# Kernel tuning notes

Hardware: AMD Instinct MI355X
Metric: run time of the kernel (lower is better)

## Reference

```python
import jax, jax.numpy as jnp
import numpy as np
from math import sqrt

B, T, C = 2, 2048, 2048
H = 16
NOPE, ROPE, VD, LORA = 128, 64, 128, 512
QK = NOPE + ROPE  # 192
EPS = 1e-6


def _make_freq_cis(T, rope_dim):
    inv = 1.0 / (10000.0 ** (np.arange(0, rope_dim, 2, dtype=np.float32) / rope_dim))
    t = np.arange(T, dtype=np.float32)
    ang = np.outer(t, inv)  # [T, rope_dim/2]
    return jnp.asarray(np.stack([np.cos(ang), np.sin(ang)], -1))  # [T, rope_dim/2, 2]


def setup_inputs() -> dict:
    key = jax.random.key(0)
    ks = jax.random.split(key, 6)
    x = jax.random.normal(ks[0], (B, T, C), jnp.float32)
    freq_cis = _make_freq_cis(T, ROPE)
    causal = jnp.where(jnp.tril(jnp.ones((T, T), bool)), 0.0, -1e9).astype(jnp.float32)
    Wq = jax.random.normal(ks[1], (C, H * QK), jnp.float32) * (1.0 / sqrt(C))
    Wckv = jax.random.normal(ks[2], (C, LORA + ROPE), jnp.float32) * (1.0 / sqrt(C))
    kv_norm_w = jnp.ones((LORA,), jnp.float32)
    Wdkv = jax.random.normal(ks[3], (LORA, H * (NOPE + VD)), jnp.float32) * (1.0 / sqrt(LORA))
    Wproj = jax.random.normal(ks[4], (H * VD, C), jnp.float32) * (1.0 / sqrt(H * VD))
    return {"x": x, "freq_cis": freq_cis, "mask": causal, "window": causal,
            "Wq": Wq, "Wckv": Wckv, "kv_norm_w": kv_norm_w, "Wdkv": Wdkv,
            "Wproj": Wproj, "start_pos": 0}


def apply_rope(x, freq_cis):
    # x: [B, T, h, D]; freq_cis: [T, D/2, 2]
    b, t, h, d = x.shape
    xr = x.reshape(b, t, h, d // 2, 2)
    fc = freq_cis.reshape(1, t, 1, d // 2, 2)
    real = xr[..., 0] * fc[..., 0] - xr[..., 1] * fc[..., 1]
    imag = xr[..., 1] * fc[..., 0] + xr[..., 0] * fc[..., 1]
    return jnp.stack([real, imag], -1).reshape(b, t, h, d)


def rms_norm(x, w, eps=EPS):
    return x * jax.lax.rsqrt(jnp.mean(x * x, -1, keepdims=True) + eps) * w


def reference(x, freq_cis, mask, window, Wq, Wckv, kv_norm_w, Wdkv, Wproj, start_pos):
    del window, start_pos  # Global attention, no KV cache (prefill)
    b, t, _ = x.shape
    q = (x @ Wq).reshape(b, t, H, QK)
    q_nope, q_rope = q[..., :NOPE], q[..., NOPE:]
    q_rope = apply_rope(q_rope, freq_cis)

    ckv = x @ Wckv  # [B, T, LORA+ROPE]
    kv_lat, k_rope = ckv[..., :LORA], ckv[..., LORA:]
    k_rope = apply_rope(k_rope.reshape(b, t, 1, ROPE), freq_cis)  # [B,T,1,ROPE]

    kv = rms_norm(kv_lat, kv_norm_w) @ Wdkv  # [B, T, H*(NOPE+VD)]
    kv = kv.reshape(b, t, H, NOPE + VD)
    k_nope, v = kv[..., :NOPE], kv[..., NOPE:]

    q = jnp.concatenate([q_nope, q_rope], -1)                                   # [B,T,H,QK]
    k = jnp.concatenate([k_nope, jnp.broadcast_to(k_rope, (b, t, H, ROPE))], -1)

    scale = 1.0 / sqrt(QK)
    atten = jnp.einsum('bqhd,bkhd->bhqk', q, k) * scale + mask  # [B,H,T,T]
    atten = jax.nn.softmax(atten, -1)
    out = jnp.einsum('bhqk,bkhd->bqhd', atten, v).reshape(b, t, H * VD)
    return out @ Wproj
```

## Files before the change

### kernel.cpp

```cpp
#include <hip/hip_runtime.h>
#include <hip/hip_bf16.h>
#include <math.h>


typedef short bf16x8 __attribute__((ext_vector_type(8)));
typedef float f32x4 __attribute__((ext_vector_type(4)));
typedef float f32x16 __attribute__((ext_vector_type(16)));

#define MFMA16(a, b, c) __builtin_amdgcn_mfma_f32_16x16x32_bf16(a, b, c, 0, 0, 0)
#define MFMA32(a, b, c) __builtin_amdgcn_mfma_f32_32x32x16_bf16(a, b, c, 0, 0, 0)

__device__ __forceinline__ short f2bf(float f) {
  union { float f; unsigned u; } v; v.f = f;
  unsigned r = v.u + 0x7fffu + ((v.u >> 16) & 1u);
  return (short)(r >> 16);
}
__device__ __forceinline__ float bf2f(short s) {
  union { unsigned u; float f; } v;
  v.u = ((unsigned)(unsigned short)s) << 16;
  return v.f;
}
__device__ __forceinline__ unsigned cvtpk(float a, float b) {
  unsigned r;
  asm("v_cvt_pk_bf16_f32 %0, %1, %2" : "=v"(r) : "v"(a), "v"(b));
  return r;
}
__device__ __forceinline__ void gl16(const void* g, void* l) {
  __builtin_amdgcn_global_load_lds(
      (const __attribute__((address_space(1))) unsigned int*)g,
      (__attribute__((address_space(3))) unsigned int*)l, 16, 0, 0);
}
#define CFENCE() asm volatile("" ::: "memory")
#define HWBAR()  do { CFENCE(); __builtin_amdgcn_s_barrier(); CFENCE(); } while (0)

__global__ __launch_bounds__(256) void cvt_k(const float* __restrict__ in,
                                             short* __restrict__ out, int n) {
  int i = (blockIdx.x * 256 + threadIdx.x) * 8;
  if (i >= n) return;
  float4 a = *(const float4*)(in + i);
  float4 b = *(const float4*)(in + i + 4);
  bf16x8 o;
  o[0] = f2bf(a.x); o[1] = f2bf(a.y); o[2] = f2bf(a.z); o[3] = f2bf(a.w);
  o[4] = f2bf(b.x); o[5] = f2bf(b.y); o[6] = f2bf(b.z); o[7] = f2bf(b.w);
  *(bf16x8*)(out + i) = o;
}

__global__ __launch_bounds__(256) void tcvt_k(const float* __restrict__ W,
                                              short* __restrict__ out,
                                              int K, int N, int Np, int row_off) {
  __shared__ float tile[32][33];
  int k0 = blockIdx.x * 32, n0 = blockIdx.y * 32;
  int tx = threadIdx.x & 31, ty = threadIdx.x >> 5;
#pragma unroll
  for (int j = 0; j < 4; j++) {
    int k = k0 + ty + j * 8, n = n0 + tx;
    tile[ty + j * 8][tx] = (n < N) ? W[(size_t)k * N + n] : 0.f;
  }
  __syncthreads();
#pragma unroll
  for (int j = 0; j < 4; j++) {
    int n = n0 + ty + j * 8;
    out[(size_t)(row_off + n) * K + k0 + tx] = f2bf(tile[tx][ty + j * 8]);
  }
}

template <int MODE, int BM, int BN, int SGL>
__global__ __launch_bounds__(512, 2) void gemm8_k(const short* __restrict__ A,
                                                  const short* __restrict__ Bt,
                                                  void* __restrict__ C1,
                                                  void* __restrict__ C2,
                                                  int M, int N, int K, int nbx) {
  constexpr int FM = BM / 32;
  constexpr int FN = BN / 64;
  constexpr int XCH = (BM * 4) / 512;
  constexpr int YCH = (BN * 4) / 512;
  __shared__ short lX[3][BM * 32];
  __shared__ short lY[3][BN * 32];

  const int nwg = gridDim.x;
  const int cpx = nwg >> 3;
  const int swz = (blockIdx.x & 7) * cpx + (blockIdx.x >> 3);
  const int bx = swz % nbx, by = swz / nbx;
  const int m0 = bx * BM, n0 = by * BN;
  const int tid = threadIdx.x, lane = tid & 63, wave = tid >> 6;
  const int wm = wave >> 2, wn = wave & 3;
  const int l15 = lane & 15, l4 = lane >> 4;
  const int nt = K >> 5;

  auto stage = [&](int t) {
    int kk = t << 5;
    short* bX = &lX[t % 3][0];
    short* bY = &lY[t % 3][0];
#pragma unroll
    for (int c = 0; c < XCH; c++) {
      int idx = c * 512 + tid;
      int row = idx >> 2, seg = idx & 3;
      gl16(A + (size_t)(m0 + row) * K + kk + ((seg ^ ((row >> 1) & 3)) << 3),
           bX + idx * 8);
    }
#pragma unroll
    for (int c = 0; c < YCH; c++) {
      int idx = c * 512 + tid;
      int row = idx >> 2, seg = idx & 3;
      gl16(Bt + (size_t)(n0 + row) * K + kk + ((seg ^ ((row >> 1) & 3)) << 3),
           bY + idx * 8);
    }
  };

  f32x4 zero = {0.f, 0.f, 0.f, 0.f};
  f32x4 acc[FM][FN];
#pragma unroll
  for (int i = 0; i < FM; i++)
#pragma unroll
    for (int j = 0; j < FN; j++) acc[i][j] = zero;

  stage(0);
  stage(1);
  if constexpr (SGL == 4) asm volatile("s_waitcnt vmcnt(4)" ::: "memory");
  else                    asm volatile("s_waitcnt vmcnt(3)" ::: "memory");
  HWBAR();

  for (int t = 0; t < nt; t++) {
    const short* bX = &lX[t % 3][0];
    const short* bY = &lY[t % 3][0];
    bf16x8 xf[FM / 2], yf[FN];
#pragma unroll
    for (int i = 0; i < FM / 2; i++) {
      int row = wm * (BM / 2) + i * 16 + l15;
      xf[i] = *(const bf16x8*)&bX[row * 32 + ((l4 ^ ((row >> 1) & 3)) << 3)];
    }
#pragma unroll
    for (int j = 0; j < FN; j++) {
      int row = wn * (BN / 4) + j * 16 + l15;
      yf[j] = *(const bf16x8*)&bY[row * 32 + ((l4 ^ ((row >> 1) & 3)) << 3)];
    }
    bool st = (t + 2 < nt);
    if (st) stage(t + 2);
    HWBAR();
    __builtin_amdgcn_sched_barrier(0);
    __builtin_amdgcn_s_setprio(1);
#pragma unroll
    for (int i = 0; i < FM / 2; i++)
#pragma unroll
      for (int j = 0; j < FN; j++) acc[i][j] = MFMA16(xf[i], yf[j], acc[i][j]);
    __builtin_amdgcn_s_setprio(0);
    bf16x8 xg[FM / 2];
#pragma unroll
    for (int i = 0; i < FM / 2; i++) {
      int row = wm * (BM / 2) + (FM / 2 + i) * 16 + l15;
      xg[i] = *(const bf16x8*)&bX[row * 32 + ((l4 ^ ((row >> 1) & 3)) << 3)];
    }
    if (st) {
      if constexpr (SGL == 4) asm volatile("s_waitcnt vmcnt(4) lgkmcnt(0)" ::: "memory");
      else                    asm volatile("s_waitcnt vmcnt(3) lgkmcnt(0)" ::: "memory");
    } else {
      asm volatile("s_waitcnt vmcnt(0) lgkmcnt(0)" ::: "memory");
    }
    HWBAR();
    __builtin_amdgcn_sched_barrier(0);
    __builtin_amdgcn_s_setprio(1);
#pragma unroll
    for (int i = 0; i < FM / 2; i++)
#pragma unroll
      for (int j = 0; j < FN; j++)
        acc[FM / 2 + i][j] = MFMA16(xg[i], yf[j], acc[FM / 2 + i][j]);
    __builtin_amdgcn_s_setprio(0);
  }

#pragma unroll
  for (int i = 0; i < FM; i++) {
#pragma unroll
    for (int j = 0; j < FN; j++) {
#pragma unroll
      for (int r = 0; r < 4; r++) {
        int m = m0 + wm * (BM / 2) + i * 16 + l4 * 4 + r;
        int n = n0 + wn * (BN / 4) + j * 16 + l15;
        if (n >= N) continue;
        float v = acc[i][j][r];
        if (MODE == 0) {
          ((short*)C1)[(size_t)m * N + n] = f2bf(v);
        } else if (MODE == 1) {
          ((float*)C1)[(size_t)m * N + n] = v;
        } else {
          int bb = m >> 11, t2 = m & 2047, hh = n >> 8, c = n & 255;
          if (c < 128)
            ((short*)C1)[((size_t)(bb * 16 + hh) * 2048 + t2) * 192 + c] = f2bf(v);
          else
            ((short*)C2)[((size_t)(bb * 16 + hh) * 128 + (c - 128)) * 2048 + t2] = f2bf(v);
        }
      }
    }
  }
}

__global__ __launch_bounds__(256) void rmsnorm_k(const short* __restrict__ qc,
                                                 const float* __restrict__ w,
                                                 short* __restrict__ out) {
  int row = blockIdx.x * 4 + (threadIdx.x >> 6);
  int lane = threadIdx.x & 63;
  const short* src = qc + (size_t)row * 3712 + 3072 + lane * 8;
  bf16x8 v = *(const bf16x8*)src;
  float f[8];
  float ss = 0.f;
#pragma unroll
  for (int j = 0; j < 8; j++) { f[j] = bf2f(v[j]); ss += f[j] * f[j]; }
#pragma unroll
  for (int m = 1; m < 64; m <<= 1) ss += __shfl_xor(ss, m);
  float r = rsqrtf(ss * (1.f / 512.f) + 1e-6f);
  bf16x8 o;
#pragma unroll
  for (int j = 0; j < 8; j++) o[j] = f2bf(f[j] * r * w[lane * 8 + j]);
  *(bf16x8*)(out + (size_t)row * 512 + lane * 8) = o;
}

__global__ __launch_bounds__(256) void qrope_k(const short* __restrict__ qc,
                                               const float* __restrict__ freq,
                                               short* __restrict__ q_all) {
  int row = blockIdx.x * 4 + (threadIdx.x >> 6);
  int lane = threadIdx.x & 63;
  int b = row >> 15, h = (row >> 11) & 15, t = row & 2047;
  const short* src = qc + (size_t)(b * 2048 + t) * 3712 + h * 192;
  short* dst = q_all + (size_t)row * 192;
  const float scale = 0.10411756f;
  dst[lane] = f2bf(bf2f(src[lane]) * scale);
  dst[lane + 64] = f2bf(bf2f(src[lane + 64]) * scale);
  int p = lane >> 1;
  float c = freq[t * 64 + p * 2], s = freq[t * 64 + p * 2 + 1];
  float x0 = bf2f(src[128 + 2 * p]), x1 = bf2f(src[128 + 2 * p + 1]);
  float v = (lane & 1) ? (x1 * c + x0 * s) : (x0 * c - x1 * s);
  dst[128 + lane] = f2bf(v * scale);
}

__global__ __launch_bounds__(64) void krope_k(const short* __restrict__ qc,
                                              const float* __restrict__ freq,
                                              short* __restrict__ k_all) {
  int bt = blockIdx.x;
  int lane = threadIdx.x;
  int b = bt >> 11, t = bt & 2047;
  const short* src = qc + (size_t)bt * 3712 + 3584;
  int p = lane >> 1;
  float c = freq[t * 64 + p * 2], s = freq[t * 64 + p * 2 + 1];
  float x0 = bf2f(src[2 * p]), x1 = bf2f(src[2 * p + 1]);
  float v = (lane & 1) ? (x1 * c + x0 * s) : (x0 * c - x1 * s);
  short vb = f2bf(v);
#pragma unroll
  for (int h = 0; h < 16; h++)
    k_all[((size_t)(b * 16 + h) * 2048 + t) * 192 + 128 + lane] = vb;
}

__device__ __forceinline__ void stage_kv4(const short* __restrict__ Kp,
                                          const short* __restrict__ VT,
                                          short* kb, short* vb, int kt, int tid) {
#pragma unroll
  for (int i = 0; i < 3; i++) {
    int idx = i * 256 + tid;
    int row = idx / 24, seg = idx % 24;
    gl16(Kp + (size_t)(kt + row) * 192 + ((seg ^ (row & 7)) << 3), kb + idx * 8);
  }
#pragma unroll
  for (int i = 0; i < 2; i++) {
    int v = i * 256 + tid;
    int row = v >> 2, seg = v & 3;
    gl16(VT + (size_t)row * 2048 + kt + ((seg ^ ((row >> 1) & 3)) << 3), vb + v * 8);
  }
}

__global__ __launch_bounds__(256) void attn_k(const short* __restrict__ q_all,
                                              const short* __restrict__ k_all,
                                              const short* __restrict__ vt,
                                              short* __restrict__ attn_out) {
  __shared__ short kbuf[2][32 * 192];
  __shared__ short vbuf[2][128 * 32];
  int bh = blockIdx.x;
  int b = bh >> 4, h = bh & 15;
  int col = gridDim.y - 1 - blockIdx.y;
  int tid = threadIdx.x;
  int wave = tid >> 6, lane = tid & 63;
  int l31 = lane & 31, hi = lane >> 5;
  int qw = col * 128 + wave * 32;
  int qrow = qw + l31;
  const short* Q = q_all + ((size_t)bh * 2048 + qrow) * 192;
  const short* Kp = k_all + (size_t)bh * 2048 * 192;
  const short* VT = vt + (size_t)bh * 128 * 2048;
  int sig = (l31 & 19) | ((l31 >> 1) & 4) | ((l31 << 1) & 8);
  int s7 = sig & 7;

  bf16x8 qf[12];
#pragma unroll
  for (int kb = 0; kb < 12; kb++)
    qf[kb] = *(const bf16x8*)(Q + kb * 16 + hi * 8);

  f32x16 o[4];
#pragma unroll
  for (int vb = 0; vb < 4; vb++)
#pragma unroll
    for (int r = 0; r < 16; r++) o[vb][r] = 0.f;
  f32x16 sInit;
#pragma unroll
  for (int r = 0; r < 16; r++) sInit[r] = -28.8539f;
  float lsum = 0.f;

  const int kend = col * 128 + 128;

  stage_kv4(Kp, VT, kbuf[0], vbuf[0], 0, tid);
  __syncthreads();

  for (int kt = 0; kt < kend; kt += 32) {
    int cur = (kt >> 5) & 1;
    if (kt + 32 < kend)
      stage_kv4(Kp, VT, kbuf[cur ^ 1], vbuf[cur ^ 1], kt + 32, tid);

    if (kt < qw + 32) {
      f32x16 sc = sInit;
#pragma unroll
      for (int kb = 0; kb < 12; kb++) {
        int c = 2 * kb + hi;
        bf16x8 kf = *(const bf16x8*)&kbuf[cur][sig * 192 + ((c ^ s7) << 3)];
        sc = MFMA32(kf, qf[kb], sc);
      }
      unsigned pw[8];
      if (kt + 32 <= qw) {
#pragma unroll
        for (int r2 = 0; r2 < 8; r2++) {
          float pa = exp2f(sc[2 * r2]);
          float pb = exp2f(sc[2 * r2 + 1]);
          lsum += pa + pb;
          pw[r2] = cvtpk(pa, pb);
        }
      } else {
#pragma unroll
        for (int r2 = 0; r2 < 8; r2++) {
          int r = 2 * r2;
          int key = kt + (r & 3) + 4 * ((r >> 2) & 1) + 8 * hi + 16 * (r >> 3);
          float va = (key <= qrow) ? sc[r] : -1e30f;
          float vb2 = (key + 1 <= qrow) ? sc[r + 1] : -1e30f;
          float pa = exp2f(va);
          float pb = exp2f(vb2);
          lsum += pa + pb;
          pw[r2] = cvtpk(pa, pb);
        }
      }
      union { unsigned u[4]; bf16x8 v; } p0, p1;
#pragma unroll
      for (int w = 0; w < 4; w++) { p0.u[w] = pw[w]; p1.u[w] = pw[4 + w]; }
#pragma unroll
      for (int vb = 0; vb < 4; vb++) {
        int vcol = vb * 32 + l31;
        int sw = (vcol >> 1) & 3;
        bf16x8 vf0 = *(const bf16x8*)&vbuf[cur][vcol * 32 + ((hi ^ sw) << 3)];
        bf16x8 vf1 = *(const bf16x8*)&vbuf[cur][vcol * 32 + (((2 + hi) ^ sw) << 3)];
        o[vb] = MFMA32(vf0, p0.v, o[vb]);
        o[vb] = MFMA32(vf1, p1.v, o[vb]);
      }
    }
    __syncthreads();
  }

  lsum += __shfl_xor(lsum, 32);
  float inv = 1.f / lsum;
  size_t base = ((size_t)b * 2048 + qrow) * 2048 + h * 128;
#pragma unroll
  for (int vb = 0; vb < 4; vb++) {
#pragma unroll
    for (int r2 = 0; r2 < 8; r2++) {
      int r = 2 * r2;
      int v = vb * 32 + (r & 3) + 8 * (r >> 2) + 4 * hi;
      unsigned pk2 = ((unsigned)(unsigned short)f2bf(o[vb][r] * inv)) |
                     (((unsigned)(unsigned short)f2bf(o[vb][r + 1] * inv)) << 16);
      *(unsigned*)(attn_out + base + v) = pk2;
    }
  }
}

extern "C" void kernel_launch(void* const* d_in, const int* in_sizes, int n_in,
                              void* d_out, int out_size, void* d_ws, size_t ws_size,
                              hipStream_t stream) {
  const float* x = (const float*)d_in[0];
  const float* freq = (const float*)d_in[1];
  const float* Wq = (const float*)d_in[4];
  const float* Wckv = (const float*)d_in[5];
  const float* kvw = (const float*)d_in[6];
  const float* Wdkv = (const float*)d_in[7];
  const float* Wproj = (const float*)d_in[8];

  char* ws = (char*)d_ws;
  size_t off = 0;
  auto alloc = [&](size_t bytes) {
    size_t o = off;
    off += (bytes + 255) & ~(size_t)255;
    return o;
  };
  size_t o_xbf = alloc(4096ull * 2048 * 2);
  size_t o_wqc = alloc(3840ull * 2048 * 2);
  size_t o_wdkv = alloc(4096ull * 512 * 2);
  size_t o_wproj = alloc(2048ull * 2048 * 2);
  size_t o_qc = alloc(4096ull * 3712 * 2);
  size_t o_kvlat = alloc(4096ull * 512 * 2);
  size_t o_qall = alloc(32ull * 2048 * 192 * 2);
  size_t o_kall = alloc(32ull * 2048 * 192 * 2);
  size_t o_vt = alloc(32ull * 128 * 2048 * 2);
  size_t o_attn = o_xbf;

  short* x_bf = (short*)(ws + o_xbf);
  short* wqc = (short*)(ws + o_wqc);
  short* wdkv = (short*)(ws + o_wdkv);
  short* wproj = (short*)(ws + o_wproj);
  short* qc = (short*)(ws + o_qc);
  short* kvlat = (short*)(ws + o_kvlat);
  short* qall = (short*)(ws + o_qall);
  short* kall = (short*)(ws + o_kall);
  short* vtb = (short*)(ws + o_vt);
  short* attnb = (short*)(ws + o_attn);

  cvt_k<<<4096, 256, 0, stream>>>(x, x_bf, 4096 * 2048);
  tcvt_k<<<dim3(64, 96), 256, 0, stream>>>(Wq, wqc, 2048, 3072, 3072, 0);
  tcvt_k<<<dim3(64, 24), 256, 0, stream>>>(Wckv, wqc, 2048, 576, 768, 3072);
  tcvt_k<<<dim3(16, 128), 256, 0, stream>>>(Wdkv, wdkv, 512, 4096, 4096, 0);
  tcvt_k<<<dim3(64, 64), 256, 0, stream>>>(Wproj, wproj, 2048, 2048, 2048, 0);

  gemm8_k<0, 256, 256, 4><<<240, 512, 0, stream>>>(x_bf, wqc, qc, nullptr,
                                                   4096, 3712, 2048, 16);

  rmsnorm_k<<<1024, 256, 0, stream>>>(qc, kvw, kvlat);
  qrope_k<<<16384, 256, 0, stream>>>(qc, freq, qall);
  krope_k<<<4096, 64, 0, stream>>>(qc, freq, kall);

  gemm8_k<2, 256, 256, 4><<<256, 512, 0, stream>>>(kvlat, wdkv, kall, vtb,
                                                   4096, 4096, 512, 16);

  attn_k<<<dim3(32, 16), 256, 0, stream>>>(qall, kall, vtb, attnb);

  gemm8_k<1, 128, 256, 3><<<256, 512, 0, stream>>>(attnb, wproj, d_out, nullptr,
                                                   4096, 2048, 2048, 32);
}
```

Before: 314.4 us.

## Double attention query tile to 256 rows with 8 waves and padded LDS

The attention kernel now uses 512 threads (8 waves) per block, each block covering 256 query rows instead of 128. Each staged K/V tile is therefore shared by twice as many waves, which halves global K/V traffic per query. The XOR-swizzled LDS layout is replaced by row padding (stride 200 for K, 40 for V) to avoid bank conflicts. The costs are a smaller grid, more wasted causal work inside each block, and some redundant loads for the padding slots.

```diff
diff --git a/kernel.cpp b/kernel.cpp
--- a/kernel.cpp
+++ b/kernel.cpp
@@ -248,42 +248,54 @@
     k_all[((size_t)(b * 16 + h) * 2048 + t) * 192 + 128 + lane] = vb;
 }
 
-__device__ __forceinline__ void stage_kv4(const short* __restrict__ Kp,
-                                          const short* __restrict__ VT,
-                                          short* kb, short* vb, int kt, int tid) {
-#pragma unroll
-  for (int i = 0; i < 3; i++) {
-    int idx = i * 256 + tid;
-    int row = idx / 24, seg = idx % 24;
-    gl16(Kp + (size_t)(kt + row) * 192 + ((seg ^ (row & 7)) << 3), kb + idx * 8);
-  }
-#pragma unroll
-  for (int i = 0; i < 2; i++) {
-    int v = i * 256 + tid;
-    int row = v >> 2, seg = v & 3;
-    gl16(VT + (size_t)row * 2048 + kt + ((seg ^ ((row >> 1) & 3)) << 3), vb + v * 8);
-  }
-}
-
-__global__ __launch_bounds__(256) void attn_k(const short* __restrict__ q_all,
-                                              const short* __restrict__ k_all,
-                                              const short* __restrict__ vt,
-                                              short* __restrict__ attn_out) {
-  __shared__ short kbuf[2][32 * 192];
-  __shared__ short vbuf[2][128 * 32];
+__device__ __forceinline__ void stage_kv8w(const short* __restrict__ Kp,
+                                           const short* __restrict__ VT,
+                                           short* kb, short* vb, int kt, int tid) {
+  {
+    int idx = tid;
+    int r = idx / 25, s = idx % 25;
+    int s2 = (s >= 24) ? 0 : s;
+    gl16(Kp + (size_t)(kt + r) * 192 + s2 * 8, kb + idx * 8);
+  }
+  if (tid < 320) {
+    int idx = 512 + tid;
+    int r = idx / 25; if (r > 31) r = 31;
+    int s = idx % 25;
+    int s2 = (s >= 24) ? 0 : s;
+    gl16(Kp + (size_t)(kt + r) * 192 + s2 * 8, kb + idx * 8);
+  }
+  {
+    int idx = tid;
+    int r = idx / 5, s = idx % 5;
+    int s2 = (s >= 4) ? 0 : s;
+    gl16(VT + (size_t)r * 2048 + kt + s2 * 8, vb + idx * 8);
+  }
+  if (tid < 128) {
+    int idx = 512 + tid;
+    int r = idx / 5, s = idx % 5;
+    int s2 = (s >= 4) ? 0 : s;
+    gl16(VT + (size_t)r * 2048 + kt + s2 * 8, vb + idx * 8);
+  }
+}
+
+__global__ __launch_bounds__(512, 2) void attn_k(const short* __restrict__ q_all,
+                                                 const short* __restrict__ k_all,
+                                                 const short* __restrict__ vt,
+                                                 short* __restrict__ attn_out) {
+  __shared__ short kbuf[2][832 * 8];
+  __shared__ short vbuf[2][128 * 40];
   int bh = blockIdx.x;
   int b = bh >> 4, h = bh & 15;
   int col = gridDim.y - 1 - blockIdx.y;
   int tid = threadIdx.x;
   int wave = tid >> 6, lane = tid & 63;
   int l31 = lane & 31, hi = lane >> 5;
-  int qw = col * 128 + wave * 32;
+  int qw = col * 256 + wave * 32;
   int qrow = qw + l31;
   const short* Q = q_all + ((size_t)bh * 2048 + qrow) * 192;
   const short* Kp = k_all + (size_t)bh * 2048 * 192;
   const short* VT = vt + (size_t)bh * 128 * 2048;
   int sig = (l31 & 19) | ((l31 >> 1) & 4) | ((l31 << 1) & 8);
-  int s7 = sig & 7;
 
   bf16x8 qf[12];
 #pragma unroll
@@ -300,22 +312,22 @@
   for (int r = 0; r < 16; r++) sInit[r] = -28.8539f;
   float lsum = 0.f;
 
-  const int kend = col * 128 + 128;
-
-  stage_kv4(Kp, VT, kbuf[0], vbuf[0], 0, tid);
+  const int kend = col * 256 + 256;
+
+  stage_kv8w(Kp, VT, kbuf[0], vbuf[0], 0, tid);
   __syncthreads();
 
   for (int kt = 0; kt < kend; kt += 32) {
     int cur = (kt >> 5) & 1;
     if (kt + 32 < kend)
-      stage_kv4(Kp, VT, kbuf[cur ^ 1], vbuf[cur ^ 1], kt + 32, tid);
+      stage_kv8w(Kp, VT, kbuf[cur ^ 1], vbuf[cur ^ 1], kt + 32, tid);
 
     if (kt < qw + 32) {
       f32x16 sc = sInit;
 #pragma unroll
       for (int kb = 0; kb < 12; kb++) {
         int c = 2 * kb + hi;
-        bf16x8 kf = *(const bf16x8*)&kbuf[cur][sig * 192 + ((c ^ s7) << 3)];
+        bf16x8 kf = *(const bf16x8*)&kbuf[cur][sig * 200 + (c << 3)];
         sc = MFMA32(kf, qf[kb], sc);
       }
       unsigned pw[8];
@@ -346,9 +358,8 @@
 #pragma unroll
       for (int vb = 0; vb < 4; vb++) {
         int vcol = vb * 32 + l31;
-        int sw = (vcol >> 1) & 3;
-        bf16x8 vf0 = *(const bf16x8*)&vbuf[cur][vcol * 32 + ((hi ^ sw) << 3)];
-        bf16x8 vf1 = *(const bf16x8*)&vbuf[cur][vcol * 32 + (((2 + hi) ^ sw) << 3)];
+        bf16x8 vf0 = *(const bf16x8*)&vbuf[cur][vcol * 40 + (hi << 3)];
+        bf16x8 vf1 = *(const bf16x8*)&vbuf[cur][vcol * 40 + ((2 + hi) << 3)];
         o[vb] = MFMA32(vf0, p0.v, o[vb]);
         o[vb] = MFMA32(vf1, p1.v, o[vb]);
       }
@@ -428,7 +439,7 @@
   gemm8_k<2, 256, 256, 4><<<256, 512, 0, stream>>>(kvlat, wdkv, kall, vtb,
                                                    4096, 4096, 512, 16);
 
-  attn_k<<<dim3(32, 16), 256, 0, stream>>>(qall, kall, vtb, attnb);
+  attn_k<<<dim3(32, 8), 512, 0, stream>>>(qall, kall, vtb, attnb);
 
   gemm8_k<1, 128, 256, 3><<<256, 512, 0, stream>>>(attnb, wproj, d_out, nullptr,
                                                    4096, 2048, 2048, 32);
```

Result: slower. 320.8 us (+2.0%).
